# Optimization experiments

Hardware: AMD Instinct MI355X
Metric: run time of the kernel (lower is better)

## Reference

```python
import jax, jax.numpy as jnp
import numpy as np

K = 3          # pooling factor (init k)
H_OUT = 8      # number of bilinear heads
H_DIM = 512    # hidden dim after pooling
BN_EPS = 1e-5
NEG_INF = -jnp.inf


def setup_inputs() -> dict:
    key = jax.random.key(0)
    ks = jax.random.split(key, 8)
    b, vn, qn, vd, qd = 16, 256, 256, 512, 768
    hk = H_DIM * K
    return {
        "v": jax.random.normal(ks[0], (b, vn, vd), jnp.float32),
        "q": jax.random.normal(ks[1], (b, qn, qd), jnp.float32),
        "Wv": jax.random.normal(ks[2], (hk, vd), jnp.float32) * 0.05,
        "bv": jax.random.normal(ks[3], (hk,), jnp.float32) * 0.05,
        "Wq": jax.random.normal(ks[4], (hk, qd), jnp.float32) * 0.05,
        "bq": jax.random.normal(ks[5], (hk,), jnp.float32) * 0.05,
        "h_mat": jax.random.normal(ks[6], (1, H_OUT, 1, hk), jnp.float32),
        "h_bias": jax.random.normal(ks[7], (1, H_OUT, 1, 1), jnp.float32),
        "bn_gamma": jnp.ones((H_DIM,), jnp.float32),
        "bn_beta": jnp.zeros((H_DIM,), jnp.float32),
    }


def _forward(v, q, Wv, bv, Wq, bq, h_mat, h_bias, bn_gamma, bn_beta):
    # FCNet (eval mode: dropout is identity; weight_norm folded into W)
    v_ = jax.nn.relu(jnp.einsum("bvd,kd->bvk", v, Wv) + bv)   # [b, vn, h_dim*k]
    q_ = jax.nn.relu(jnp.einsum("bqd,kd->bqk", q, Wq) + bq)   # [b, qn, h_dim*k]

    # Bilinear attention maps: [b, h_out, vn, qn]
    att = jnp.einsum("xhyk,bvk,bqk->bhvq", h_mat, v_, q_) + h_bias

    # v_mask / q_mask (all-zero token rows masked to -inf)
    v_zero = jnp.sum(jnp.abs(v), axis=2) == 0                  # [b, vn]
    q_zero = jnp.sum(jnp.abs(q), axis=2) == 0                  # [b, qn]
    att = jnp.where(v_zero[:, None, :, None], NEG_INF, att)
    att = jnp.where(q_zero[:, None, None, :], NEG_INF, att)

    # Fused per-head attention pooling, summed over heads (original Python loop)
    fused = jnp.einsum("bhvq,bqk->bhvk", att, q_)
    logits_k = jnp.einsum("bvk,bhvk->bk", v_, fused)           # [b, h_dim*k]

    # AvgPool1d(k, stride=k) * k  == sum over groups of k
    b = logits_k.shape[0]
    logits = logits_k.reshape(b, H_DIM, K).sum(axis=2)         # [b, h_dim]

    # BatchNorm1d (training-mode batch statistics, biased variance)
    mu = logits.mean(axis=0)
    var = logits.var(axis=0)
    logits = (logits - mu) * jax.lax.rsqrt(var + BN_EPS) * bn_gamma + bn_beta
    return logits, att


def reference(v, q, Wv, bv, Wq, bq, h_mat, h_bias, bn_gamma, bn_beta):
    return _forward(v, q, Wv, bv, Wq, bq, h_mat, h_bias, bn_gamma, bn_beta)
```

## Files before the change

kernel.cpp:

```cpp
#include <hip/hip_runtime.h>
#include <math.h>

#define BB    16
#define VN    256
#define QN    256
#define VD    512
#define QD    768
#define HK    1536
#define HDIM  512

typedef _Float16 half8 __attribute__((ext_vector_type(8)));
typedef _Float16 half4 __attribute__((ext_vector_type(4)));
typedef float f32x4 __attribute__((ext_vector_type(4)));

__global__ __launch_bounds__(256) void conv_mask2(
    const float* __restrict__ v, const float* __restrict__ q,
    _Float16* __restrict__ v16, _Float16* __restrict__ q16,
    float* __restrict__ vz, float* __restrict__ qz) {
    int which = blockIdx.y;
    const float* src = which ? q : v;
    _Float16* dst = which ? q16 : v16;
    float* outz = which ? qz : vz;
    int D = which ? QD : VD;
    int w = threadIdx.x >> 6, ln = threadIdx.x & 63;
    int row = blockIdx.x * 4 + w;
    const float* p = src + (size_t)row * D;
    _Float16* d = dst + (size_t)row * D;
    float s = 0.f;
    for (int c = ln * 4; c < D; c += 256) {
        float4 x = *(const float4*)(p + c);
        s += fabsf(x.x) + fabsf(x.y) + fabsf(x.z) + fabsf(x.w);
        half4 hh = {(_Float16)x.x, (_Float16)x.y, (_Float16)x.z, (_Float16)x.w};
        *(half4*)(d + c) = hh;
    }
    for (int off = 32; off > 0; off >>= 1) s += __shfl_down(s, off);
    if (ln == 0) outz[row] = (s == 0.f) ? 1.f : 0.f;
}

__global__ __launch_bounds__(256) void conv_w3(
    const float* __restrict__ Wv, _Float16* __restrict__ Wv16, int n4v,
    const float* __restrict__ Wq, _Float16* __restrict__ Wq16, int n4q,
    const float* __restrict__ hm, _Float16* __restrict__ hs16) {
    if (blockIdx.y == 2) {
        int k = blockIdx.x * 256 + threadIdx.x;
        if (k >= HK) return;
        float s = 0.f;
#pragma unroll
        for (int h = 0; h < 8; ++h) {
            float x = hm[h * HK + k];
            s += x;
            hs16[h * HK + k] = (_Float16)x;
        }
        hs16[8 * HK + k] = (_Float16)s;
        return;
    }
    const float* src = blockIdx.y ? Wq : Wv;
    _Float16* dst = blockIdx.y ? Wq16 : Wv16;
    int n4 = blockIdx.y ? n4q : n4v;
    int i = blockIdx.x * 256 + threadIdx.x;
    if (i < n4) {
        float4 x = ((const float4*)src)[i];
        half4 h = {(_Float16)x.x, (_Float16)x.y, (_Float16)x.z, (_Float16)x.w};
        ((half4*)dst)[i] = h;
    }
}

__global__ __launch_bounds__(128) void proj_lds(
    const _Float16* __restrict__ Ain, const _Float16* __restrict__ W16,
    const float* __restrict__ bias, _Float16* __restrict__ C16, int K) {
    __shared__ _Float16 As[64 * 64];
    __shared__ _Float16 Bs[64 * 64];
    int m0 = blockIdx.y * 64, n0 = blockIdx.x * 64;
    int t = threadIdx.x;
    int w = t >> 6, ln = t & 63, quad = ln >> 4, r16 = ln & 15;
    int arow = t >> 3, aseg = t & 7;
    int sg = aseg ^ (arow & 7);
    const _Float16* ApG = Ain + (size_t)(m0 + arow) * K + aseg * 8;
    const _Float16* BpG = W16 + (size_t)(n0 + arow) * K + aseg * 8;
    half8 ra[4], rb[4];
#pragma unroll
    for (int c = 0; c < 4; ++c) {
        ra[c] = *(const half8*)(ApG + (size_t)c * 16 * K);
        rb[c] = *(const half8*)(BpG + (size_t)c * 16 * K);
    }
    f32x4 acc[2][4] = {};
    for (int k0 = 0; k0 < K; k0 += 64) {
        __syncthreads();
#pragma unroll
        for (int c = 0; c < 4; ++c) {
            *(half8*)&As[(c * 16 + arow) * 64 + sg * 8] = ra[c];
            *(half8*)&Bs[(c * 16 + arow) * 64 + sg * 8] = rb[c];
        }
        __syncthreads();
        if (k0 + 64 < K) {
#pragma unroll
            for (int c = 0; c < 4; ++c) {
                ra[c] = *(const half8*)(ApG + (size_t)c * 16 * K + k0 + 64);
                rb[c] = *(const half8*)(BpG + (size_t)c * 16 * K + k0 + 64);
            }
        }
#pragma unroll
        for (int kc = 0; kc < 2; ++kc) {
            half8 af[2], bf[4];
#pragma unroll
            for (int fi = 0; fi < 2; ++fi) {
                int rl = w * 32 + fi * 16 + r16;
                af[fi] = *(const half8*)&As[rl * 64 + ((kc * 4 + quad) ^ (rl & 7)) * 8];
            }
#pragma unroll
            for (int fj = 0; fj < 4; ++fj) {
                int rl = fj * 16 + r16;
                bf[fj] = *(const half8*)&Bs[rl * 64 + ((kc * 4 + quad) ^ (rl & 7)) * 8];
            }
#pragma unroll
            for (int fi = 0; fi < 2; ++fi)
#pragma unroll
                for (int fj = 0; fj < 4; ++fj)
                    acc[fi][fj] = __builtin_amdgcn_mfma_f32_16x16x32_f16(
                        af[fi], bf[fj], acc[fi][fj], 0, 0, 0);
        }
    }
#pragma unroll
    for (int fi = 0; fi < 2; ++fi) {
#pragma unroll
        for (int r = 0; r < 4; ++r) {
            int m = m0 + w * 32 + fi * 16 + quad * 4 + r;
#pragma unroll
            for (int fj = 0; fj < 4; ++fj) {
                int n = n0 + fj * 16 + r16;
                float x = acc[fi][fj][r] + bias[n];
                C16[(size_t)m * HK + n] = (_Float16)fmaxf(x, 0.f);
            }
        }
    }
}

__global__ __launch_bounds__(128, 2) void att8(
    const _Float16* __restrict__ v16, const _Float16* __restrict__ q16,
    const _Float16* __restrict__ hs16, const float* __restrict__ hb,
    const float* __restrict__ vz, const float* __restrict__ qz,
    float* __restrict__ att_out, _Float16* __restrict__ A16) {
    __shared__ _Float16 As[64 * 64];
    __shared__ _Float16 Bs[32 * 64];
    __shared__ _Float16 Hl[8 * HK];
    int b = blockIdx.z;
    int i0 = blockIdx.y * 64, j0 = blockIdx.x * 32;
    int t = threadIdx.x;
    int w = t >> 6, ln = t & 63, quad = ln >> 4, r16 = ln & 15;
    int arow = t >> 3, aseg = t & 7;
    int sg = aseg ^ (arow & 7);
    for (int u = t * 8; u < 8 * HK; u += 128 * 8)
        *(half8*)&Hl[u] = *(const half8*)(hs16 + u);
    const _Float16* ApG = v16 + (size_t)b * VN * HK + (size_t)(i0 + arow) * HK + aseg * 8;
    const _Float16* BpG = q16 + (size_t)b * QN * HK + (size_t)(j0 + arow) * HK + aseg * 8;
    half8 ra[4], rb[2];
#pragma unroll
    for (int c = 0; c < 4; ++c)
        ra[c] = *(const half8*)(ApG + (size_t)c * 16 * HK);
#pragma unroll
    for (int c = 0; c < 2; ++c)
        rb[c] = *(const half8*)(BpG + (size_t)c * 16 * HK);
    f32x4 acc[8][2][2] = {};
    for (int it = 0; it < 24; ++it) {
        __syncthreads();
#pragma unroll
        for (int c = 0; c < 4; ++c)
            *(half8*)&As[(c * 16 + arow) * 64 + sg * 8] = ra[c];
#pragma unroll
        for (int c = 0; c < 2; ++c)
            *(half8*)&Bs[(c * 16 + arow) * 64 + sg * 8] = rb[c];
        __syncthreads();
        if (it + 1 < 24) {
            int kn = (it + 1) * 64;
#pragma unroll
            for (int c = 0; c < 4; ++c)
                ra[c] = *(const half8*)(ApG + (size_t)c * 16 * HK + kn);
#pragma unroll
            for (int c = 0; c < 2; ++c)
                rb[c] = *(const half8*)(BpG + (size_t)c * 16 * HK + kn);
        }
        int kb = it * 64;
#pragma unroll
        for (int kc = 0; kc < 2; ++kc) {
            half8 af[2], bf[2];
#pragma unroll
            for (int fi = 0; fi < 2; ++fi) {
                int rl = w * 32 + fi * 16 + r16;
                af[fi] = *(const half8*)&As[rl * 64 + ((kc * 4 + quad) ^ (rl & 7)) * 8];
            }
#pragma unroll
            for (int fj = 0; fj < 2; ++fj) {
                int rl = fj * 16 + r16;
                bf[fj] = *(const half8*)&Bs[rl * 64 + ((kc * 4 + quad) ^ (rl & 7)) * 8];
            }
#pragma unroll
            for (int hh = 0; hh < 8; ++hh) {
                half8 hmv = *(const half8*)&Hl[hh * HK + kb + (kc * 4 + quad) * 8];
#pragma unroll
                for (int fi = 0; fi < 2; ++fi) {
                    half8 am = af[fi] * hmv;
#pragma unroll
                    for (int fj = 0; fj < 2; ++fj)
                        acc[hh][fi][fj] = __builtin_amdgcn_mfma_f32_16x16x32_f16(
                            am, bf[fj], acc[hh][fi][fj], 0, 0, 0);
                }
            }
        }
    }
    float hbs[8];
    float hbsum = 0.f;
#pragma unroll
    for (int h = 0; h < 8; ++h) {
        hbs[h] = hb[h];
        hbsum += hbs[h];
    }
    float qm[2];
#pragma unroll
    for (int fj = 0; fj < 2; ++fj)
        qm[fj] = qz[b * QN + j0 + fj * 16 + r16];
#pragma unroll
    for (int fi = 0; fi < 2; ++fi) {
#pragma unroll
        for (int r = 0; r < 4; ++r) {
            int i = i0 + w * 32 + fi * 16 + quad * 4 + r;
            float vm = vz[b * VN + i];
#pragma unroll
            for (int fj = 0; fj < 2; ++fj) {
                int j = j0 + fj * 16 + r16;
                bool msk = (vm != 0.f) || (qm[fj] != 0.f);
                float s = 0.f;
#pragma unroll
                for (int h = 0; h < 8; ++h) {
                    float a = acc[h][fi][fj][r];
                    s += a;
                    float x = a + hbs[h];
                    if (msk) x = -INFINITY;
                    att_out[((size_t)(b * 8 + h)) * VN * QN + (size_t)i * QN + j] = x;
                }
                float xs = s + hbsum;
                if (msk) xs = -INFINITY;
                A16[(size_t)b * VN * QN + (size_t)i * QN + j] = (_Float16)xs;
            }
        }
    }
}

__global__ __launch_bounds__(256) void transpose_q16(const _Float16* __restrict__ q16,
                                                     _Float16* __restrict__ q16t) {
    __shared__ _Float16 Ls[32][72];
    int b = blockIdx.z;
    int k0 = blockIdx.x * 64, j0 = blockIdx.y * 32;
    int t = threadIdx.x;
    const _Float16* src = q16 + (size_t)b * QN * HK;
    int tj = t >> 3, tk = (t & 7) * 8;
    half8 vv = *(const half8*)(src + (size_t)(j0 + tj) * HK + k0 + tk);
#pragma unroll
    for (int e = 0; e < 8; ++e) Ls[tj][tk + e] = vv[e];
    __syncthreads();
    int ok = t >> 2, oj = (t & 3) * 8;
    half8 ov;
#pragma unroll
    for (int e = 0; e < 8; ++e) ov[e] = Ls[oj + e][ok];
    *(half8*)(q16t + (size_t)b * HK * QN + (size_t)(k0 + ok) * QN + j0 + oj) = ov;
}

__global__ __launch_bounds__(256) void t_lk_mfma(
    const _Float16* __restrict__ A16, const _Float16* __restrict__ q16t,
    const _Float16* __restrict__ v16, float* __restrict__ lk) {
    __shared__ _Float16 As[256 * 32];
    __shared__ _Float16 Bs[64 * 32];
    __shared__ float red[16][64];
    int b = blockIdx.y;
    int k0 = blockIdx.x * 64;
    int t = threadIdx.x;
    int w = t >> 6, ln = t & 63, quad = ln >> 4, r16 = ln & 15;
    const _Float16* Ab = A16 + (size_t)b * VN * QN;
    const _Float16* Qt = q16t + (size_t)b * HK * QN + (size_t)k0 * QN;
    int ar = t >> 2, aseg = t & 3;
    f32x4 acc[4][4] = {};
    for (int j0 = 0; j0 < QN; j0 += 32) {
        half8 a0 = *(const half8*)(Ab + (size_t)(ar +   0) * QN + j0 + aseg * 8);
        half8 a1 = *(const half8*)(Ab + (size_t)(ar +  64) * QN + j0 + aseg * 8);
        half8 a2 = *(const half8*)(Ab + (size_t)(ar + 128) * QN + j0 + aseg * 8);
        half8 a3 = *(const half8*)(Ab + (size_t)(ar + 192) * QN + j0 + aseg * 8);
        half8 bv = *(const half8*)(Qt + (size_t)ar * QN + j0 + aseg * 8);
        __syncthreads();
        *(half8*)&As[(ar +   0) * 32 + aseg * 8] = a0;
        *(half8*)&As[(ar +  64) * 32 + aseg * 8] = a1;
        *(half8*)&As[(ar + 128) * 32 + aseg * 8] = a2;
        *(half8*)&As[(ar + 192) * 32 + aseg * 8] = a3;
        *(half8*)&Bs[ar * 32 + aseg * 8] = bv;
        __syncthreads();
        half8 af[4], bf[4];
#pragma unroll
        for (int fi = 0; fi < 4; ++fi)
            af[fi] = *(const half8*)&As[(w * 64 + fi * 16 + r16) * 32 + quad * 8];
#pragma unroll
        for (int fj = 0; fj < 4; ++fj)
            bf[fj] = *(const half8*)&Bs[(fj * 16 + r16) * 32 + quad * 8];
#pragma unroll
        for (int fi = 0; fi < 4; ++fi)
#pragma unroll
            for (int fj = 0; fj < 4; ++fj)
                acc[fi][fj] = __builtin_amdgcn_mfma_f32_16x16x32_f16(
                    af[fi], bf[fj], acc[fi][fj], 0, 0, 0);
    }
    const _Float16* Vb = v16 + (size_t)b * VN * HK;
    float part[4] = {0.f, 0.f, 0.f, 0.f};
#pragma unroll
    for (int fi = 0; fi < 4; ++fi) {
#pragma unroll
        for (int r = 0; r < 4; ++r) {
            int i = w * 64 + fi * 16 + quad * 4 + r;
#pragma unroll
            for (int fj = 0; fj < 4; ++fj) {
                float vv = (float)Vb[(size_t)i * HK + k0 + fj * 16 + r16];
                part[fj] += acc[fi][fj][r] * vv;
            }
        }
    }
#pragma unroll
    for (int fj = 0; fj < 4; ++fj)
        red[w * 4 + quad][fj * 16 + r16] = part[fj];
    __syncthreads();
    if (t < 64) {
        float s = 0.f;
#pragma unroll
        for (int g = 0; g < 16; ++g) s += red[g][t];
        lk[b * HK + k0 + t] = s;
    }
}

__global__ __launch_bounds__(256) void bn_kernel(
    const float* __restrict__ lk, const float* __restrict__ gamma,
    const float* __restrict__ beta, float* __restrict__ out) {
    int d = blockIdx.x * blockDim.x + threadIdx.x;
    if (d >= HDIM) return;
    float l[BB];
    float mu = 0.f;
#pragma unroll
    for (int b = 0; b < BB; ++b) {
        const float* p = lk + b * HK + 3 * d;
        float s = p[0] + p[1] + p[2];
        l[b] = s;
        mu += s;
    }
    mu *= (1.f / BB);
    float var = 0.f;
#pragma unroll
    for (int b = 0; b < BB; ++b) {
        float dd = l[b] - mu;
        var += dd * dd;
    }
    var *= (1.f / BB);
    float inv = rsqrtf(var + 1e-5f);
    float g = gamma[d], be = beta[d];
#pragma unroll
    for (int b = 0; b < BB; ++b)
        out[b * HDIM + d] = (l[b] - mu) * inv * g + be;
}

extern "C" void kernel_launch(void* const* d_in, const int* in_sizes, int n_in,
                              void* d_out, int out_size, void* d_ws, size_t ws_size,
                              hipStream_t stream) {
    const float* v  = (const float*)d_in[0];
    const float* q  = (const float*)d_in[1];
    const float* Wv = (const float*)d_in[2];
    const float* bv = (const float*)d_in[3];
    const float* Wq = (const float*)d_in[4];
    const float* bq = (const float*)d_in[5];
    const float* hm = (const float*)d_in[6];
    const float* hb = (const float*)d_in[7];
    const float* gamma = (const float*)d_in[8];
    const float* beta  = (const float*)d_in[9];

    float* out_logits = (float*)d_out;
    float* out_att    = out_logits + BB * HDIM;

    _Float16* h = (_Float16*)d_ws;
    _Float16* v16   = h;
    _Float16* q16   = v16 + (size_t)BB * VN * HK;
    _Float16* q16t  = q16 + (size_t)BB * QN * HK;
    _Float16* A16   = q16t + (size_t)BB * HK * QN;
    _Float16* v16in = A16 + (size_t)BB * VN * QN;
    _Float16* q16in = v16in + (size_t)BB * VN * VD;
    _Float16* Wv16  = q16in + (size_t)BB * QN * QD;
    _Float16* Wq16  = Wv16 + (size_t)HK * VD;
    _Float16* hs16  = Wq16 + (size_t)HK * QD;
    float* lk = (float*)(hs16 + 9 * HK + 8);
    float* vz = lk + BB * HK;
    float* qz = vz + BB * VN;

    conv_mask2<<<dim3(BB * VN / 4, 2), 256, 0, stream>>>(v, q, v16in, q16in, vz, qz);
    conv_w3<<<dim3((HK * QD / 4 + 255) / 256, 3), 256, 0, stream>>>(
        Wv, Wv16, HK * VD / 4, Wq, Wq16, HK * QD / 4, hm, hs16);

    proj_lds<<<dim3(HK / 64, BB * VN / 64), 128, 0, stream>>>(v16in, Wv16, bv, v16, VD);
    proj_lds<<<dim3(HK / 64, BB * QN / 64), 128, 0, stream>>>(q16in, Wq16, bq, q16, QD);

    att8<<<dim3(QN / 32, VN / 64, BB), 128, 0, stream>>>(
        v16, q16, hs16, hb, vz, qz, out_att, A16);

    transpose_q16<<<dim3(HK / 64, QN / 32, BB), 256, 0, stream>>>(q16, q16t);

    t_lk_mfma<<<dim3(HK / 64, BB), 256, 0, stream>>>(A16, q16t, v16, lk);

    bn_kernel<<<dim3((HDIM + 255) / 256), 256, 0, stream>>>(lk, gamma, beta, out_logits);
}
```

Before: 198.8 us.

## Split attention heads across waves in att kernel with LDS head-sum reduction

After: 195.2 us. About the same (-1.8%).

```diff
diff --git a/kernel.cpp b/kernel.cpp
--- a/kernel.cpp
+++ b/kernel.cpp
@@ -135,7 +135,7 @@
     }
 }
 
-__global__ __launch_bounds__(128, 2) void att8(
+__global__ __launch_bounds__(256, 2) void att42(
     const _Float16* __restrict__ v16, const _Float16* __restrict__ q16,
     const _Float16* __restrict__ hs16, const float* __restrict__ hb,
     const float* __restrict__ vz, const float* __restrict__ qz,
@@ -147,37 +147,29 @@
     int i0 = blockIdx.y * 64, j0 = blockIdx.x * 32;
     int t = threadIdx.x;
     int w = t >> 6, ln = t & 63, quad = ln >> 4, r16 = ln & 15;
-    int arow = t >> 3, aseg = t & 7;
-    int sg = aseg ^ (arow & 7);
-    for (int u = t * 8; u < 8 * HK; u += 128 * 8)
+    int iw = w & 1, hg = w >> 1, h0 = hg * 4;
+    int arow = t >> 2, as0 = t & 3;
+    int brow = t >> 3, bs0 = t & 7;
+    for (int u = t * 8; u < 8 * HK; u += 256 * 8)
         *(half8*)&Hl[u] = *(const half8*)(hs16 + u);
-    const _Float16* ApG = v16 + (size_t)b * VN * HK + (size_t)(i0 + arow) * HK + aseg * 8;
-    const _Float16* BpG = q16 + (size_t)b * QN * HK + (size_t)(j0 + arow) * HK + aseg * 8;
-    half8 ra[4], rb[2];
-#pragma unroll
-    for (int c = 0; c < 4; ++c)
-        ra[c] = *(const half8*)(ApG + (size_t)c * 16 * HK);
-#pragma unroll
-    for (int c = 0; c < 2; ++c)
-        rb[c] = *(const half8*)(BpG + (size_t)c * 16 * HK);
-    f32x4 acc[8][2][2] = {};
+    const _Float16* ApG = v16 + (size_t)b * VN * HK + (size_t)(i0 + arow) * HK;
+    const _Float16* BpG = q16 + (size_t)b * QN * HK + (size_t)(j0 + brow) * HK;
+    half8 ra[2], rb;
+    ra[0] = *(const half8*)(ApG + as0 * 8);
+    ra[1] = *(const half8*)(ApG + as0 * 8 + 32);
+    rb    = *(const half8*)(BpG + bs0 * 8);
+    f32x4 acc[4][2][2] = {};
     for (int it = 0; it < 24; ++it) {
         __syncthreads();
-#pragma unroll
-        for (int c = 0; c < 4; ++c)
-            *(half8*)&As[(c * 16 + arow) * 64 + sg * 8] = ra[c];
-#pragma unroll
-        for (int c = 0; c < 2; ++c)
-            *(half8*)&Bs[(c * 16 + arow) * 64 + sg * 8] = rb[c];
+        *(half8*)&As[arow * 64 + ((as0    ) ^ (arow & 7)) * 8] = ra[0];
+        *(half8*)&As[arow * 64 + ((as0 + 4) ^ (arow & 7)) * 8] = ra[1];
+        *(half8*)&Bs[brow * 64 + ((bs0    ) ^ (brow & 7)) * 8] = rb;
         __syncthreads();
         if (it + 1 < 24) {
             int kn = (it + 1) * 64;
-#pragma unroll
-            for (int c = 0; c < 4; ++c)
-                ra[c] = *(const half8*)(ApG + (size_t)c * 16 * HK + kn);
-#pragma unroll
-            for (int c = 0; c < 2; ++c)
-                rb[c] = *(const half8*)(BpG + (size_t)c * 16 * HK + kn);
+            ra[0] = *(const half8*)(ApG + kn + as0 * 8);
+            ra[1] = *(const half8*)(ApG + kn + as0 * 8 + 32);
+            rb    = *(const half8*)(BpG + kn + bs0 * 8);
         }
         int kb = it * 64;
 #pragma unroll
@@ -185,7 +177,7 @@
             half8 af[2], bf[2];
 #pragma unroll
             for (int fi = 0; fi < 2; ++fi) {
-                int rl = w * 32 + fi * 16 + r16;
+                int rl = iw * 32 + fi * 16 + r16;
                 af[fi] = *(const half8*)&As[rl * 64 + ((kc * 4 + quad) ^ (rl & 7)) * 8];
             }
 #pragma unroll
@@ -194,8 +186,8 @@
                 bf[fj] = *(const half8*)&Bs[rl * 64 + ((kc * 4 + quad) ^ (rl & 7)) * 8];
             }
 #pragma unroll
-            for (int hh = 0; hh < 8; ++hh) {
-                half8 hmv = *(const half8*)&Hl[hh * HK + kb + (kc * 4 + quad) * 8];
+            for (int hh = 0; hh < 4; ++hh) {
+                half8 hmv = *(const half8*)&Hl[(h0 + hh) * HK + kb + (kc * 4 + quad) * 8];
 #pragma unroll
                 for (int fi = 0; fi < 2; ++fi) {
                     half8 am = af[fi] * hmv;
@@ -207,39 +199,77 @@
             }
         }
     }
-    float hbs[8];
+    float s[2][2][4];
+#pragma unroll
+    for (int fi = 0; fi < 2; ++fi)
+#pragma unroll
+        for (int fj = 0; fj < 2; ++fj)
+#pragma unroll
+            for (int r = 0; r < 4; ++r) {
+                float ss = 0.f;
+#pragma unroll
+                for (int hh = 0; hh < 4; ++hh) ss += acc[hh][fi][fj][r];
+                s[fi][fj][r] = ss;
+            }
+    float hbv[4];
+#pragma unroll
+    for (int hh = 0; hh < 4; ++hh) hbv[hh] = hb[h0 + hh];
     float hbsum = 0.f;
 #pragma unroll
-    for (int h = 0; h < 8; ++h) {
-        hbs[h] = hb[h];
-        hbsum += hbs[h];
-    }
+    for (int h = 0; h < 8; ++h) hbsum += hb[h];
     float qm[2];
 #pragma unroll
-    for (int fj = 0; fj < 2; ++fj)
-        qm[fj] = qz[b * QN + j0 + fj * 16 + r16];
+    for (int fj = 0; fj < 2; ++fj) qm[fj] = qz[b * QN + j0 + fj * 16 + r16];
+    float* outb = att_out + (size_t)b * 8 * VN * QN;
 #pragma unroll
     for (int fi = 0; fi < 2; ++fi) {
 #pragma unroll
         for (int r = 0; r < 4; ++r) {
-            int i = i0 + w * 32 + fi * 16 + quad * 4 + r;
+            int i = i0 + iw * 32 + fi * 16 + quad * 4 + r;
             float vm = vz[b * VN + i];
 #pragma unroll
             for (int fj = 0; fj < 2; ++fj) {
                 int j = j0 + fj * 16 + r16;
                 bool msk = (vm != 0.f) || (qm[fj] != 0.f);
-                float s = 0.f;
-#pragma unroll
-                for (int h = 0; h < 8; ++h) {
-                    float a = acc[h][fi][fj][r];
-                    s += a;
-                    float x = a + hbs[h];
+#pragma unroll
+                for (int hh = 0; hh < 4; ++hh) {
+                    float x = acc[hh][fi][fj][r] + hbv[hh];
                     if (msk) x = -INFINITY;
-                    att_out[((size_t)(b * 8 + h)) * VN * QN + (size_t)i * QN + j] = x;
+                    outb[(size_t)(h0 + hh) * VN * QN + (size_t)i * QN + j] = x;
                 }
-                float xs = s + hbsum;
-                if (msk) xs = -INFINITY;
-                A16[(size_t)b * VN * QN + (size_t)i * QN + j] = (_Float16)xs;
+            }
+        }
+    }
+    __syncthreads();
+    float* Red = (float*)As;
+    if (hg) {
+#pragma unroll
+        for (int fi = 0; fi < 2; ++fi)
+#pragma unroll
+            for (int fj = 0; fj < 2; ++fj)
+#pragma unroll
+                for (int r = 0; r < 4; ++r)
+                    Red[iw * 1024 + (fi * 16 + quad * 4 + r) * 32 + fj * 16 + r16] =
+                        s[fi][fj][r];
+    }
+    __syncthreads();
+    if (!hg) {
+        _Float16* Ab = A16 + (size_t)b * VN * QN;
+#pragma unroll
+        for (int fi = 0; fi < 2; ++fi) {
+#pragma unroll
+            for (int r = 0; r < 4; ++r) {
+                int i = i0 + iw * 32 + fi * 16 + quad * 4 + r;
+                float vm = vz[b * VN + i];
+#pragma unroll
+                for (int fj = 0; fj < 2; ++fj) {
+                    int j = j0 + fj * 16 + r16;
+                    float tot = s[fi][fj][r] +
+                                Red[iw * 1024 + (fi * 16 + quad * 4 + r) * 32 + fj * 16 + r16] +
+                                hbsum;
+                    if (vm != 0.f || qm[fj] != 0.f) tot = -INFINITY;
+                    Ab[(size_t)i * QN + j] = (_Float16)tot;
+                }
             }
         }
     }
@@ -398,7 +428,7 @@
     proj_lds<<<dim3(HK / 64, BB * VN / 64), 128, 0, stream>>>(v16in, Wv16, bv, v16, VD);
     proj_lds<<<dim3(HK / 64, BB * QN / 64), 128, 0, stream>>>(q16in, Wq16, bq, q16, QD);
 
-    att8<<<dim3(QN / 32, VN / 64, BB), 128, 0, stream>>>(
+    att42<<<dim3(QN / 32, VN / 64, BB), 256, 0, stream>>>(
         v16, q16, hs16, hb, vz, qz, out_att, A16);
 
     transpose_q16<<<dim3(HK / 64, QN / 32, BB), 256, 0, stream>>>(q16, q16t);
```
